# Performance work log

Hardware: AMD Instinct MI355X
Metric: run time of the kernel (lower is better)

Reference implementation:

```python
import jax, jax.numpy as jnp
import numpy as np

BATCH, C_IN, C_OUT, H, K = 32, 128, 256, 56, 3

def setup_inputs() -> dict:
    key = jax.random.key(0)
    k1, k2 = jax.random.split(key)
    img = jax.random.normal(k1, (BATCH, C_IN, H, H), dtype=jnp.float32)
    # matches nn.Parameter((rand - 0.5) * (1 / (C_IN * K**2)))
    filtro = (jax.random.uniform(k2, (C_OUT, C_IN, K, K), dtype=jnp.float32) - 0.5) * (1.0 / (C_IN * K * K))
    return {"img": img, "filtro": filtro}

def reference(img, filtro):
    # Original: padding=0 (stride=1), im2col unfold + matmul == VALID cross-correlation.
    return jax.lax.conv_general_dilated(
        img, filtro,
        window_strides=(1, 1),
        padding="VALID",
        dimension_numbers=("NCHW", "OIHW", "NCHW"),
    )  # -> [BATCH, C_OUT, H-K+1, H-K+1]
```

## Files before the change

kernel.cpp:

```cpp
#include <hip/hip_runtime.h>


#define BB   32
#define CIN  128
#define COUT 256
#define HH   56
#define WW   56
#define OH   54
#define OW   54

typedef short bf16x8 __attribute__((ext_vector_type(8)));
typedef float f32x4  __attribute__((ext_vector_type(4)));
typedef unsigned short u16x8 __attribute__((ext_vector_type(8)));

#define GLOAD_LDS16(g, l) __builtin_amdgcn_global_load_lds( \
    (const __attribute__((address_space(1))) unsigned int*)(g), \
    (__attribute__((address_space(3))) unsigned int*)(l), 16, 0, 0)

static __device__ __forceinline__ unsigned short f2bf(float f) {
    unsigned int u = __float_as_uint(f);
    u += 0x7FFFu + ((u >> 16) & 1u);
    return (unsigned short)(u >> 16);
}

__global__ __launch_bounds__(256) void prep_img(const float* __restrict__ img,
                                                unsigned short* __restrict__ imgT) {
    const int b = blockIdx.x / HH;
    const int y = blockIdx.x - b * HH;
    for (int i = threadIdx.x; i < 16 * WW; i += 256) {
        const int g = i / WW;
        const int x = i - g * WW;
        unsigned short pk[8];
        #pragma unroll
        for (int j = 0; j < 8; ++j)
            pk[j] = f2bf(img[((size_t)(b * CIN + g * 8 + j) * HH + y) * WW + x]);
        *(u16x8*)(imgT + ((size_t)(b * HH + y) * WW + x) * CIN + g * 8) = *(u16x8*)pk;
    }
}

__global__ __launch_bounds__(256) void prep_flt(const float* __restrict__ flt,
                                                unsigned short* __restrict__ filtG) {
    const int idx = blockIdx.x * 256 + threadIdx.x;
    const int co = idx >> 7;
    const int ci = idx & 127;
    const int cot = co >> 7, col = co & 127;
    const int c = ci >> 5, kg = (ci >> 3) & 3, e = ci & 7;
    const size_t base = (size_t)(cot * 4 + c) * 36864 + kg * 1024 + col * 8 + e;
    #pragma unroll
    for (int t = 0; t < 9; ++t)
        filtG[base + t * 4096] = f2bf(flt[(size_t)(co * CIN + ci) * 9 + t]);
}

#define IMG_ROWB  896
#define IMG_PLANE 8960
#define IMG_BUF   35840
#define FLTA_OFF  71680
#define FLTB_OFF  112640
#define LDS_BYTES 145408

template<int T0, int NT>
static __device__ __forceinline__ void compute_taps(const char* __restrict__ aR,
                                                    const char* __restrict__ bBc,
                                                    f32x4 (&acc)[4][7]) {
    #pragma unroll
    for (int tt = 0; tt < NT; ++tt) {
        const int t = T0 + tt;
        const int dy = t / 3, dx = t % 3;
        bf16x8 A[4];
        #pragma unroll
        for (int cf = 0; cf < 4; ++cf)
            A[cf] = *(const bf16x8*)(aR + tt * 8192 + cf * 256);
        #pragma unroll
        for (int xo = 0; xo < 7; ++xo) {
            bf16x8 bv = *(const bf16x8*)(bBc + dy * IMG_ROWB + (xo * 8 + dx) * 16);
            #pragma unroll
            for (int cf = 0; cf < 4; ++cf)
                acc[cf][xo] = __builtin_amdgcn_mfma_f32_16x16x32_bf16(A[cf], bv, acc[cf][xo], 0, 0, 0);
        }
    }
}

__global__ __launch_bounds__(512, 1) void conv_mfma(
    const unsigned short* __restrict__ imgT,
    const unsigned short* __restrict__ filtG,
    float* __restrict__ out)
{
    __shared__ char lds[LDS_BYTES];

    const int tid  = threadIdx.x;
    const int lane = tid & 63, w8 = tid >> 6;
    const int ch   = w8 >> 2, rp = w8 & 3;
    const int sub  = lane & 15, kg = lane >> 4;
    const int sr   = sub >> 3,  sc = sub & 7;

    const int w    = (blockIdx.x & 7) * 56 + (blockIdx.x >> 3);
    const int cot  = w & 1;
    const int rest = w >> 1;
    const int strip = rest % 7;
    const int b     = rest / 7;
    const int co0   = cot * 128;
    const int ystart = (strip < 6) ? strip * 8 : (OH - 8);

    char* const pImg = lds;
    char* const pFA  = lds + FLTA_OFF;
    char* const pFB  = lds + FLTB_OFF;
    const char* bB = pImg + kg * IMG_PLANE + (rp * 2 + sr) * IMG_ROWB + sc * 16;
    const char* aA = pFA + kg * 2048 + (ch * 64 + sub) * 16;
    const char* aB = pFB + kg * 2048 + (ch * 64 + sub) * 16;

    const unsigned short* fsrc = filtG + (size_t)cot * 147456;

    const int hs = tid >> 8, t8 = tid & 255;
    int goffI[3];
    #pragma unroll
    for (int k = 0; k < 3; ++k) {
        const int s = k * 256 + t8;
        const int r = s / 56;
        const int x = s - r * 56;
        goffI[k] = ((b * HH + ystart + r) * WW + x) * CIN + hs * 8;
    }
    const bool act2 = (t8 < 48);

    #define STAGE_FA(cn) do { \
        _Pragma("unroll") \
        for (int k = 0; k < 5; ++k) \
            GLOAD_LDS16(fsrc + (cn) * 36864 + (k * 512 + tid) * 8, \
                        pFA + (k * 512 + tid) * 16); \
    } while (0)
    #define STAGE_FB(cn) do { \
        _Pragma("unroll") \
        for (int k = 0; k < 4; ++k) \
            GLOAD_LDS16(fsrc + (cn) * 36864 + 20480 + (k * 512 + tid) * 8, \
                        pFB + (k * 512 + tid) * 16); \
    } while (0)
    #define STAGE_I01(cn) do { \
        char* d_ = pImg + ((cn) & 1) * IMG_BUF + hs * IMG_PLANE; \
        _Pragma("unroll") \
        for (int k = 0; k < 3; ++k) \
            if (k < 2 || act2) \
                GLOAD_LDS16(imgT + goffI[k] + (cn) * 32, d_ + (k * 256 + t8) * 16); \
    } while (0)
    #define STAGE_I23(cn) do { \
        char* d_ = pImg + ((cn) & 1) * IMG_BUF + (2 + hs) * IMG_PLANE; \
        _Pragma("unroll") \
        for (int k = 0; k < 3; ++k) \
            if (k < 2 || act2) \
                GLOAD_LDS16(imgT + goffI[k] + (cn) * 32 + 16, d_ + (k * 256 + t8) * 16); \
    } while (0)
    #define PHASE_SYNC() do { \
        asm volatile("s_waitcnt vmcnt(0) lgkmcnt(0)" ::: "memory"); \
        __builtin_amdgcn_s_barrier(); \
        __builtin_amdgcn_sched_barrier(0); \
    } while (0)

    f32x4 acc[4][7];
    #pragma unroll
    for (int cf = 0; cf < 4; ++cf)
        #pragma unroll
        for (int xo = 0; xo < 7; ++xo) acc[cf][xo] = (f32x4)0.0f;

    STAGE_FA(0);
    STAGE_I01(0);
    STAGE_I23(0);
    PHASE_SYNC();

    #define CONV_ITER(C) do { \
         \
        STAGE_FB(C); \
        if ((C) < 3) STAGE_I01((C) + 1); \
        { const char* bBc = bB + ((C) & 1) * IMG_BUF; \
          __builtin_amdgcn_s_setprio(1); \
          compute_taps<0, 5>(aA, bBc, acc); \
          __builtin_amdgcn_s_setprio(0); } \
        PHASE_SYNC(); \
         \
        if ((C) < 3) { STAGE_FA((C) + 1); STAGE_I23((C) + 1); } \
        { const char* bBc = bB + ((C) & 1) * IMG_BUF; \
          __builtin_amdgcn_s_setprio(1); \
          compute_taps<5, 4>(aB, bBc, acc); \
          __builtin_amdgcn_s_setprio(0); } \
        if ((C) < 3) PHASE_SYNC(); \
    } while (0)

    CONV_ITER(0);
    CONV_ITER(1);
    CONV_ITER(2);
    CONV_ITER(3);

    const int y = ystart + rp * 2 + sr;
    #pragma unroll
    for (int cf = 0; cf < 4; ++cf) {
        const int cob = co0 + ch * 64 + cf * 16 + kg * 4;
        #pragma unroll
        for (int xo = 0; xo < 7; ++xo) {
            const int x = xo * 8 + sc;
            if (x < OW) {
                float* o = out + ((size_t)(b * COUT + cob) * OH + y) * OW + x;
                #pragma unroll
                for (int j = 0; j < 4; ++j)
                    o[(size_t)j * OH * OW] = acc[cf][xo][j];
            }
        }
    }
}

#define COB  16
#define THF  6
#define CIBF 2
#define IRF  (THF + 2)
__global__ __launch_bounds__(256) void conv3x3_fp32(
    const float* __restrict__ img, const float* __restrict__ flt,
    float* __restrict__ out)
{
    __shared__ float si[CIBF][IRF][WW];
    __shared__ float sf[CIBF][COB][9];
    const int tid = threadIdx.x;
    const int tx  = tid & 63;
    const int tg  = tid >> 6;
    int bid = blockIdx.x;
    const int ytile = bid % (OH / THF);  bid /= (OH / THF);
    const int cob   = bid % (COUT / COB); bid /= (COUT / COB);
    const int b     = bid;
    const int y0  = ytile * THF;
    const int co0 = cob * COB;
    float acc[4][THF];
    #pragma unroll
    for (int c = 0; c < 4; ++c)
        #pragma unroll
        for (int y = 0; y < THF; ++y) acc[c][y] = 0.0f;
    for (int ci0 = 0; ci0 < CIN; ci0 += CIBF) {
        for (int i = tid; i < CIBF * IRF * (WW / 4); i += 256) {
            const int cil = i / (IRF * (WW / 4));
            int rem = i - cil * (IRF * (WW / 4));
            const int r = rem / (WW / 4);
            const int v = rem - r * (WW / 4);
            const float4* src = reinterpret_cast<const float4*>(
                img + (((size_t)b * CIN + (ci0 + cil)) * HH + (y0 + r)) * WW) + v;
            reinterpret_cast<float4*>(&si[cil][r][0])[v] = *src;
        }
        for (int i = tid; i < CIBF * COB * 9; i += 256) {
            const int cil = i / (COB * 9);
            int rem = i - cil * (COB * 9);
            const int col = rem / 9;
            const int e   = rem - col * 9;
            sf[cil][col][e] = flt[(((size_t)(co0 + col)) * CIN + (ci0 + cil)) * 9 + e];
        }
        __syncthreads();
        if (tx < OW) {
            #pragma unroll
            for (int cil = 0; cil < CIBF; ++cil) {
                float f[4][9];
                #pragma unroll
                for (int c = 0; c < 4; ++c)
                    #pragma unroll
                    for (int e = 0; e < 9; ++e) f[c][e] = sf[cil][tg * 4 + c][e];
                float a[IRF][3];
                #pragma unroll
                for (int r = 0; r < IRF; ++r) {
                    a[r][0] = si[cil][r][tx + 0];
                    a[r][1] = si[cil][r][tx + 1];
                    a[r][2] = si[cil][r][tx + 2];
                }
                #pragma unroll
                for (int y = 0; y < THF; ++y)
                    #pragma unroll
                    for (int dy = 0; dy < 3; ++dy)
                        #pragma unroll
                        for (int c = 0; c < 4; ++c)
                            acc[c][y] = fmaf(a[y + dy][0], f[c][dy * 3 + 0],
                                        fmaf(a[y + dy][1], f[c][dy * 3 + 1],
                                        fmaf(a[y + dy][2], f[c][dy * 3 + 2], acc[c][y])));
            }
        }
        __syncthreads();
    }
    if (tx < OW) {
        #pragma unroll
        for (int c = 0; c < 4; ++c) {
            const int co = co0 + tg * 4 + c;
            #pragma unroll
            for (int y = 0; y < THF; ++y)
                out[(((size_t)b * COUT + co) * OH + (y0 + y)) * OW + tx] = acc[c][y];
        }
    }
}

extern "C" void kernel_launch(void* const* d_in, const int* in_sizes, int n_in,
                              void* d_out, int out_size, void* d_ws, size_t ws_size,
                              hipStream_t stream) {
    const float* img = (const float*)d_in[0];
    const float* flt = (const float*)d_in[1];
    float* out = (float*)d_out;

    const size_t IMGT_BYTES = (size_t)BB * HH * WW * CIN * 2;
    const size_t FILT_BYTES = (size_t)2 * 4 * 36864 * 2;
    if (ws_size < IMGT_BYTES + FILT_BYTES) {
        conv3x3_fp32<<<BB * (COUT / COB) * (OH / THF), 256, 0, stream>>>(img, flt, out);
        return;
    }
    unsigned short* imgT  = (unsigned short*)d_ws;
    unsigned short* filtG = (unsigned short*)((char*)d_ws + IMGT_BYTES);

    prep_img<<<BB * HH, 256, 0, stream>>>(img, imgT);
    prep_flt<<<(COUT * CIN) / 256, 256, 0, stream>>>(flt, filtG);
    conv_mfma<<<2 * 7 * BB, 512, 0, stream>>>(imgT, filtG, out);
}
```

Before: 94.57 us.

## Reuse image rows across ky taps via DPP rotation, regroup filter by kx

Reorders the filter layout so taps are grouped by kx column, and for each kx loads the ky=0 and ky=2 image fragments once from LDS. The ky=1 fragment is synthesised in registers with a DPP row-rotate by 8 lanes plus a select, which cuts LDS reads for the B operand by a third. The filter staging split between the A and B buffers changes from 5/4 taps to 6/3, with the FB offset moved to match. The cost is extra VALU/DPP work and higher register pressure from holding 14 B fragments.

```diff
diff --git a/kernel.cpp b/kernel.cpp
--- a/kernel.cpp
+++ b/kernel.cpp
@@ -45,38 +45,88 @@
     const int ci = idx & 127;
     const int cot = co >> 7, col = co & 127;
     const int c = ci >> 5, kg = (ci >> 3) & 3, e = ci & 7;
-    const size_t base = (size_t)(cot * 4 + c) * 36864 + kg * 1024 + col * 8 + e;
-    #pragma unroll
-    for (int t = 0; t < 9; ++t)
-        filtG[base + t * 4096] = f2bf(flt[(size_t)(co * CIN + ci) * 9 + t]);
+    const size_t blk = (size_t)(cot * 4 + c) * 36864 + kg * 1024 + col * 8 + e;
+    #pragma unroll
+    for (int t = 0; t < 9; ++t) {
+        const int ky = t / 3, kx = t % 3;
+        const int off = (kx < 2) ? (kx * 3 + ky) * 4096 : 24576 + ky * 4096;
+        filtG[blk + off] = f2bf(flt[(size_t)(co * CIN + ci) * 9 + t]);
+    }
 }
 
 #define IMG_ROWB  896
 #define IMG_PLANE 8960
 #define IMG_BUF   35840
 #define FLTA_OFF  71680
-#define FLTB_OFF  112640
+#define FLTB_OFF  120832
 #define LDS_BYTES 145408
 
-template<int T0, int NT>
-static __device__ __forceinline__ void compute_taps(const char* __restrict__ aR,
-                                                    const char* __restrict__ bBc,
-                                                    f32x4 (&acc)[4][7]) {
-    #pragma unroll
-    for (int tt = 0; tt < NT; ++tt) {
-        const int t = T0 + tt;
-        const int dy = t / 3, dx = t % 3;
+static __device__ __forceinline__ int dpp_ror8(int x) {
+    return __builtin_amdgcn_update_dpp(0, x, 0x128, 0xF, 0xF, true);
+}
+static __device__ __forceinline__ bf16x8 rot8(bf16x8 v) {
+    union { bf16x8 h; int i[4]; } u, r;
+    u.h = v;
+    #pragma unroll
+    for (int k = 0; k < 4; ++k) r.i[k] = dpp_ror8(u.i[k]);
+    return r.h;
+}
+static __device__ __forceinline__ bf16x8 sel8(bool c0, bf16x8 a, bf16x8 b) {
+    union { bf16x8 h; int i[4]; } ua, ub, o;
+    ua.h = a; ub.h = b;
+    #pragma unroll
+    for (int k = 0; k < 4; ++k) o.i[k] = c0 ? ua.i[k] : ub.i[k];
+    return o.h;
+}
+
+template<int DX, int S>
+static __device__ __forceinline__ void do_dxg(const char* __restrict__ aR,
+                                              const char* __restrict__ bBc,
+                                              const bool sr0,
+                                              f32x4 (&acc)[4][7])
+{
+    bf16x8 b0[7], b2[7];
+    #pragma unroll
+    for (int xo = 0; xo < 7; ++xo)
+        b0[xo] = *(const bf16x8*)(bBc + (xo * 8 + DX) * 16);
+    #pragma unroll
+    for (int xo = 0; xo < 7; ++xo)
+        b2[xo] = *(const bf16x8*)(bBc + 2 * IMG_ROWB + (xo * 8 + DX) * 16);
+
+    {
         bf16x8 A[4];
         #pragma unroll
         for (int cf = 0; cf < 4; ++cf)
-            A[cf] = *(const bf16x8*)(aR + tt * 8192 + cf * 256);
+            A[cf] = *(const bf16x8*)(aR + (S + 0) * 8192 + cf * 256);
+        #pragma unroll
+        for (int xo = 0; xo < 7; ++xo)
+            #pragma unroll
+            for (int cf = 0; cf < 4; ++cf)
+                acc[cf][xo] = __builtin_amdgcn_mfma_f32_16x16x32_bf16(A[cf], b0[xo], acc[cf][xo], 0, 0, 0);
+    }
+    {
+        bf16x8 A[4];
+        #pragma unroll
+        for (int cf = 0; cf < 4; ++cf)
+            A[cf] = *(const bf16x8*)(aR + (S + 1) * 8192 + cf * 256);
         #pragma unroll
         for (int xo = 0; xo < 7; ++xo) {
-            bf16x8 bv = *(const bf16x8*)(bBc + dy * IMG_ROWB + (xo * 8 + dx) * 16);
+            bf16x8 b1 = sel8(sr0, rot8(b0[xo]), rot8(b2[xo]));
             #pragma unroll
             for (int cf = 0; cf < 4; ++cf)
-                acc[cf][xo] = __builtin_amdgcn_mfma_f32_16x16x32_bf16(A[cf], bv, acc[cf][xo], 0, 0, 0);
-        }
+                acc[cf][xo] = __builtin_amdgcn_mfma_f32_16x16x32_bf16(A[cf], b1, acc[cf][xo], 0, 0, 0);
+        }
+    }
+    {
+        bf16x8 A[4];
+        #pragma unroll
+        for (int cf = 0; cf < 4; ++cf)
+            A[cf] = *(const bf16x8*)(aR + (S + 2) * 8192 + cf * 256);
+        #pragma unroll
+        for (int xo = 0; xo < 7; ++xo)
+            #pragma unroll
+            for (int cf = 0; cf < 4; ++cf)
+                acc[cf][xo] = __builtin_amdgcn_mfma_f32_16x16x32_bf16(A[cf], b2[xo], acc[cf][xo], 0, 0, 0);
     }
 }
 
@@ -92,6 +142,7 @@
     const int ch   = w8 >> 2, rp = w8 & 3;
     const int sub  = lane & 15, kg = lane >> 4;
     const int sr   = sub >> 3,  sc = sub & 7;
+    const bool sr0 = (sr == 0);
 
     const int w    = (blockIdx.x & 7) * 56 + (blockIdx.x >> 3);
     const int cot  = w & 1;
@@ -123,14 +174,14 @@
 
     #define STAGE_FA(cn) do { \
         _Pragma("unroll") \
-        for (int k = 0; k < 5; ++k) \
+        for (int k = 0; k < 6; ++k) \
             GLOAD_LDS16(fsrc + (cn) * 36864 + (k * 512 + tid) * 8, \
                         pFA + (k * 512 + tid) * 16); \
     } while (0)
     #define STAGE_FB(cn) do { \
         _Pragma("unroll") \
-        for (int k = 0; k < 4; ++k) \
-            GLOAD_LDS16(fsrc + (cn) * 36864 + 20480 + (k * 512 + tid) * 8, \
+        for (int k = 0; k < 3; ++k) \
+            GLOAD_LDS16(fsrc + (cn) * 36864 + 24576 + (k * 512 + tid) * 8, \
                         pFB + (k * 512 + tid) * 16); \
     } while (0)
     #define STAGE_I01(cn) do { \
@@ -170,14 +221,15 @@
         if ((C) < 3) STAGE_I01((C) + 1); \
         { const char* bBc = bB + ((C) & 1) * IMG_BUF; \
           __builtin_amdgcn_s_setprio(1); \
-          compute_taps<0, 5>(aA, bBc, acc); \
+          do_dxg<0, 0>(aA, bBc, sr0, acc); \
+          do_dxg<1, 3>(aA, bBc, sr0, acc); \
           __builtin_amdgcn_s_setprio(0); } \
         PHASE_SYNC(); \
          \
         if ((C) < 3) { STAGE_FA((C) + 1); STAGE_I23((C) + 1); } \
         { const char* bBc = bB + ((C) & 1) * IMG_BUF; \
           __builtin_amdgcn_s_setprio(1); \
-          compute_taps<5, 4>(aB, bBc, acc); \
+          do_dxg<2, 0>(aB, bBc, sr0, acc); \
           __builtin_amdgcn_s_setprio(0); } \
         if ((C) < 3) PHASE_SYNC(); \
     } while (0)
```

Result: no change. 96.16 us (+1.7%).

## Fuse image fp32-to-bf16 transpose into conv kernel via register staging

Applied to the files above, without the earlier changes.

Removes the separate prep_img pass that wrote a transposed bf16 copy of the image to workspace. The conv kernel now loads fp32 NCHW pixels directly into registers, prefetched one chunk ahead, then converts them to bf16 and writes them into the LDS tile layout. This saves a full write and re-read of the intermediate image and one kernel launch. In exchange it uses 64 extra registers per thread, issues many scalar strided global loads instead of 16-byte async LDS loads, and each of the two co-tiles reads and converts the fp32 image redundantly.

```diff
diff --git a/kernel.cpp b/kernel.cpp
--- a/kernel.cpp
+++ b/kernel.cpp
@@ -8,6 +8,7 @@
 #define WW   56
 #define OH   54
 #define OW   54
+#define HW   3136
 
 typedef short bf16x8 __attribute__((ext_vector_type(8)));
 typedef float f32x4  __attribute__((ext_vector_type(4)));
@@ -21,21 +22,6 @@
     unsigned int u = __float_as_uint(f);
     u += 0x7FFFu + ((u >> 16) & 1u);
     return (unsigned short)(u >> 16);
-}
-
-__global__ __launch_bounds__(256) void prep_img(const float* __restrict__ img,
-                                                unsigned short* __restrict__ imgT) {
-    const int b = blockIdx.x / HH;
-    const int y = blockIdx.x - b * HH;
-    for (int i = threadIdx.x; i < 16 * WW; i += 256) {
-        const int g = i / WW;
-        const int x = i - g * WW;
-        unsigned short pk[8];
-        #pragma unroll
-        for (int j = 0; j < 8; ++j)
-            pk[j] = f2bf(img[((size_t)(b * CIN + g * 8 + j) * HH + y) * WW + x]);
-        *(u16x8*)(imgT + ((size_t)(b * HH + y) * WW + x) * CIN + g * 8) = *(u16x8*)pk;
-    }
 }
 
 __global__ __launch_bounds__(256) void prep_flt(const float* __restrict__ flt,
@@ -80,8 +66,8 @@
     }
 }
 
-__global__ __launch_bounds__(512, 1) void conv_mfma(
-    const unsigned short* __restrict__ imgT,
+__global__ __launch_bounds__(512, 1) void conv_fused(
+    const float* __restrict__ imgF,
     const unsigned short* __restrict__ filtG,
     float* __restrict__ out)
 {
@@ -110,17 +96,46 @@
 
     const unsigned short* fsrc = filtG + (size_t)cot * 147456;
 
-    const int hs = tid >> 8, t8 = tid & 255;
-    int goffI[3];
-    #pragma unroll
-    for (int k = 0; k < 3; ++k) {
-        const int s = k * 256 + t8;
-        const int r = s / 56;
-        const int x = s - r * 56;
-        goffI[k] = ((b * HH + ystart + r) * WW + x) * CIN + hs * 8;
-    }
-    const bool act2 = (t8 < 48);
-
+    const int s1 = tid;
+    const bool has2 = (tid < 48);
+    const int s2 = 512 + tid;
+    int gb1, gb2;
+    {
+        const int r = s1 / 56, x = s1 - r * 56;
+        gb1 = b * (CIN * HW) + (ystart + r) * WW + x;
+    }
+    {
+        const int r = s2 / 56, x = s2 - r * 56;
+        gb2 = b * (CIN * HW) + (ystart + r) * WW + x;
+    }
+
+    #define LOADI(cn) do { \
+        _Pragma("unroll") \
+        for (int q = 0; q < 32; ++q) st1[q] = imgF[gb1 + ((cn) * 32 + q) * HW]; \
+        if (has2) { \
+            _Pragma("unroll") \
+            for (int q = 0; q < 32; ++q) st2[q] = imgF[gb2 + ((cn) * 32 + q) * HW]; \
+        } \
+    } while (0)
+    #define WRITEI(cn) do { \
+        char* d_ = pImg + ((cn) & 1) * IMG_BUF; \
+        _Pragma("unroll") \
+        for (int g_ = 0; g_ < 4; ++g_) { \
+            unsigned short h_[8]; \
+            _Pragma("unroll") \
+            for (int e_ = 0; e_ < 8; ++e_) h_[e_] = f2bf(st1[g_ * 8 + e_]); \
+            *(u16x8*)(d_ + g_ * IMG_PLANE + s1 * 16) = *(u16x8*)h_; \
+        } \
+        if (has2) { \
+            _Pragma("unroll") \
+            for (int g_ = 0; g_ < 4; ++g_) { \
+                unsigned short h_[8]; \
+                _Pragma("unroll") \
+                for (int e_ = 0; e_ < 8; ++e_) h_[e_] = f2bf(st2[g_ * 8 + e_]); \
+                *(u16x8*)(d_ + g_ * IMG_PLANE + s2 * 16) = *(u16x8*)h_; \
+            } \
+        } \
+    } while (0)
     #define STAGE_FA(cn) do { \
         _Pragma("unroll") \
         for (int k = 0; k < 5; ++k) \
@@ -133,20 +148,6 @@
             GLOAD_LDS16(fsrc + (cn) * 36864 + 20480 + (k * 512 + tid) * 8, \
                         pFB + (k * 512 + tid) * 16); \
     } while (0)
-    #define STAGE_I01(cn) do { \
-        char* d_ = pImg + ((cn) & 1) * IMG_BUF + hs * IMG_PLANE; \
-        _Pragma("unroll") \
-        for (int k = 0; k < 3; ++k) \
-            if (k < 2 || act2) \
-                GLOAD_LDS16(imgT + goffI[k] + (cn) * 32, d_ + (k * 256 + t8) * 16); \
-    } while (0)
-    #define STAGE_I23(cn) do { \
-        char* d_ = pImg + ((cn) & 1) * IMG_BUF + (2 + hs) * IMG_PLANE; \
-        _Pragma("unroll") \
-        for (int k = 0; k < 3; ++k) \
-            if (k < 2 || act2) \
-                GLOAD_LDS16(imgT + goffI[k] + (cn) * 32 + 16, d_ + (k * 256 + t8) * 16); \
-    } while (0)
     #define PHASE_SYNC() do { \
         asm volatile("s_waitcnt vmcnt(0) lgkmcnt(0)" ::: "memory"); \
         __builtin_amdgcn_s_barrier(); \
@@ -159,22 +160,23 @@
         #pragma unroll
         for (int xo = 0; xo < 7; ++xo) acc[cf][xo] = (f32x4)0.0f;
 
+    float st1[32], st2[32];
+
+    LOADI(0);
     STAGE_FA(0);
-    STAGE_I01(0);
-    STAGE_I23(0);
+    asm volatile("s_waitcnt vmcnt(0)" ::: "memory");
+    WRITEI(0);
     PHASE_SYNC();
 
     #define CONV_ITER(C) do { \
-         \
+        if ((C) < 3) LOADI((C) + 1); \
         STAGE_FB(C); \
-        if ((C) < 3) STAGE_I01((C) + 1); \
         { const char* bBc = bB + ((C) & 1) * IMG_BUF; \
           __builtin_amdgcn_s_setprio(1); \
           compute_taps<0, 5>(aA, bBc, acc); \
           __builtin_amdgcn_s_setprio(0); } \
         PHASE_SYNC(); \
-         \
-        if ((C) < 3) { STAGE_FA((C) + 1); STAGE_I23((C) + 1); } \
+        if ((C) < 3) { WRITEI((C) + 1); STAGE_FA((C) + 1); } \
         { const char* bBc = bB + ((C) & 1) * IMG_BUF; \
           __builtin_amdgcn_s_setprio(1); \
           compute_taps<5, 4>(aB, bBc, acc); \
@@ -292,16 +294,13 @@
     const float* flt = (const float*)d_in[1];
     float* out = (float*)d_out;
 
-    const size_t IMGT_BYTES = (size_t)BB * HH * WW * CIN * 2;
     const size_t FILT_BYTES = (size_t)2 * 4 * 36864 * 2;
-    if (ws_size < IMGT_BYTES + FILT_BYTES) {
+    if (ws_size < FILT_BYTES) {
         conv3x3_fp32<<<BB * (COUT / COB) * (OH / THF), 256, 0, stream>>>(img, flt, out);
         return;
     }
-    unsigned short* imgT  = (unsigned short*)d_ws;
-    unsigned short* filtG = (unsigned short*)((char*)d_ws + IMGT_BYTES);
-
-    prep_img<<<BB * HH, 256, 0, stream>>>(img, imgT);
+    unsigned short* filtG = (unsigned short*)d_ws;
+
     prep_flt<<<(COUT * CIN) / 256, 256, 0, stream>>>(flt, filtG);
-    conv_mfma<<<2 * 7 * BB, 512, 0, stream>>>(imgT, filtG, out);
-}
+    conv_fused<<<2 * 7 * BB, 512, 0, stream>>>(img, filtG, out);
+}
```

Measured after the change: 133.1 us. +40.7%, slower.
